# Kernel tuning notes

Measured on AMD Instinct MI355X. Metric: run time of the kernel, lower is better.

## Reference

```python
import jax, jax.numpy as jnp
import numpy as np
from jax import lax

D, NH, T, DFF, SD = 8, 4, 60, 2048, 17
DH = D // NH
NEG = -1e9

def _ln(x, g, b, eps=1e-5):
    m = jnp.mean(x, -1, keepdims=True)
    v = jnp.mean((x - m) ** 2, -1, keepdims=True)
    return (x - m) / jnp.sqrt(v + eps) * g + b

def _mha(q_in, k_in, v_in, Wqkv, bqkv, Wo, bo, mask):
    Wq, Wk, Wv = jnp.split(Wqkv, 3, axis=0)
    bq, bk, bv = jnp.split(bqkv, 3)
    def proj(x, W, bb):
        B, S, _ = x.shape
        return (x @ W.T + bb).reshape(B, S, NH, DH).transpose(0, 2, 1, 3)
    q = proj(q_in, Wq, bq); k = proj(k_in, Wk, bk); v = proj(v_in, Wv, bv)
    s = jnp.einsum('bhqd,bhkd->bhqk', q, k) / np.float32(np.sqrt(DH))
    s = jnp.where(mask, NEG, s)
    o = jnp.einsum('bhqk,bhkd->bhqd', jax.nn.softmax(s, axis=-1), v)
    B, _, S, _ = o.shape
    return o.transpose(0, 2, 1, 3).reshape(B, S, D) @ Wo.T + bo

def _ffn(x, W1, b1, W2, b2):
    return jax.nn.relu(x @ W1.T + b1) @ W2.T + b2

def _forward(x, emb_W, emb_b, eqW, eqb, eoW, eob, ef1W, ef1b, ef2W, ef2b, el1g, el1b, el2g, el2b, eng, enb, dsqW, dsqb, dsoW, dsob, dcqW, dcqb, dcoW, dcob, df1W, df1b, df2W, df2b, dl1g, dl1b, dl2g, dl2b, dl3g, dl3b, dng, dnb, fc_W, fc_b):
    B = x.shape[0]
    idx = jnp.arange(T)
    causal = (idx[None, :] > idx[:, None])[None, None]  # [1,1,T,T], True = blocked

    @jax.checkpoint
    def step(buf, t):
        keymask = (idx > t)[None, None, None, :]  # positions beyond t are padding
        mem = buf
        for i in range(6):  # nn.Transformer default encoder layers
            mem = _ln(mem + _mha(mem, mem, mem, eqW[i], eqb[i], eoW[i], eob[i], keymask), el1g[i], el1b[i])
            mem = _ln(mem + _ffn(mem, ef1W[i], ef1b[i], ef2W[i], ef2b[i]), el2g[i], el2b[i])
        mem = _ln(mem, eng, enb)
        y = buf
        for i in range(2):  # decoder layers
            y = _ln(y + _mha(y, y, y, dsqW[i], dsqb[i], dsoW[i], dsob[i], causal), dl1g[i], dl1b[i])
            y = _ln(y + _mha(y, mem, mem, dcqW[i], dcqb[i], dcoW[i], dcob[i], keymask), dl2g[i], dl2b[i])
            y = _ln(y + _ffn(y, df1W[i], df1b[i], df2W[i], df2b[i]), dl3g[i], dl3b[i])
        y = _ln(y, dng, dnb)
        st = jnp.take(y, t, axis=1) @ fc_W.T + fc_b  # decoded state at last valid pos [B,17]
        buf = buf.at[:, t + 1].set(st @ emb_W.T + emb_b, mode='drop')
        return buf, st

    buf0 = jnp.zeros((B, T, D), x.dtype).at[:, 0].set(x)
    _, states = lax.scan(step, buf0, idx)
    return jnp.transpose(states, (1, 0, 2))  # [B, T, state_dim]

def setup_inputs() -> dict:
    B = 128
    keys = iter(jax.random.split(jax.random.key(0), 64))
    def W(shape):
        return jax.random.normal(next(keys), shape, jnp.float32) / np.float32(np.sqrt(shape[-1]))
    z = lambda *s: jnp.zeros(s, jnp.float32)
    o = lambda *s: jnp.ones(s, jnp.float32)
    return dict(
        quantized_eos_embedding=jax.random.normal(next(keys), (B, D), jnp.float32),
        emb_W=W((D, SD)), emb_b=z(D),
        eqW=W((6, 3 * D, D)), eqb=z(6, 3 * D), eoW=W((6, D, D)), eob=z(6, D),
        ef1W=W((6, DFF, D)), ef1b=z(6, DFF), ef2W=W((6, D, DFF)), ef2b=z(6, D),
        el1g=o(6, D), el1b=z(6, D), el2g=o(6, D), el2b=z(6, D), eng=o(D), enb=z(D),
        dsqW=W((2, 3 * D, D)), dsqb=z(2, 3 * D), dsoW=W((2, D, D)), dsob=z(2, D),
        dcqW=W((2, 3 * D, D)), dcqb=z(2, 3 * D), dcoW=W((2, D, D)), dcob=z(2, D),
        df1W=W((2, DFF, D)), df1b=z(2, DFF), df2W=W((2, D, DFF)), df2b=z(2, D),
        dl1g=o(2, D), dl1b=z(2, D), dl2g=o(2, D), dl2b=z(2, D), dl3g=o(2, D), dl3b=z(2, D),
        dng=o(D), dnb=z(D),
        fc_W=W((SD, D)), fc_b=z(SD),
    )

def reference(quantized_eos_embedding, emb_W, emb_b, eqW, eqb, eoW, eob, ef1W, ef1b, ef2W, ef2b, el1g, el1b, el2g, el2b, eng, enb, dsqW, dsqb, dsoW, dsob, dcqW, dcqb, dcoW, dcob, df1W, df1b, df2W, df2b, dl1g, dl1b, dl2g, dl2b, dl3g, dl3b, dng, dnb, fc_W, fc_b):
    return _forward(quantized_eos_embedding, emb_W, emb_b, eqW, eqb, eoW, eob, ef1W, ef1b, ef2W, ef2b, el1g, el1b, el2g, el2b, eng, enb, dsqW, dsqb, dsoW, dsob, dcqW, dcqb, dcoW, dcob, df1W, df1b, df2W, df2b, dl1g, dl1b, dl2g, dl2b, dl3g, dl3b, dng, dnb, fc_W, fc_b)
```

## Files before the change

### kernel.cpp

```cpp
#include <hip/hip_runtime.h>


typedef __attribute__((ext_vector_type(8))) short short8;
typedef __attribute__((ext_vector_type(4))) float floatx4;
typedef __attribute__((ext_vector_type(4))) unsigned uint4v;

#define DEV static __device__ __forceinline__

namespace {
constexpr int D   = 8;
constexpr int T   = 60;
constexpr int DFF = 2048;
constexpr int SD  = 17;
constexpr int NT  = 512;
constexpr int NW  = NT / 64;
constexpr int NBLK = DFF / 32;
constexpr int BPW  = NBLK / NW;
constexpr int LSTR = NBLK * 2048;
}

struct Params { const float* in[39]; float* out; };

DEV unsigned short f2bf(float f) {
  unsigned u = __builtin_bit_cast(unsigned, f);
  return (unsigned short)((u + 0x8000u) >> 16);
}
DEV float bf2f(unsigned short h) {
  unsigned u = ((unsigned)h) << 16;
  return __builtin_bit_cast(float, u);
}
DEV floatx4 mfma16(short8 a, short8 b, floatx4 c) {
  return __builtin_amdgcn_mfma_f32_16x16x32_bf16(a, b, c, 0, 0, 0);
}
DEV unsigned cvtpk(float lo, float hi) {
  unsigned r;
  asm("v_cvt_pk_bf16_f32 %0, %1, %2" : "=v"(r) : "v"(lo), "v"(hi));
  return r;
}
DEV float lo2f(unsigned u) { return __builtin_bit_cast(float, u << 16); }
DEV float hi2f(unsigned u) { return __builtin_bit_cast(float, u & 0xffff0000u); }
DEV short8 pack4(unsigned a, unsigned b, unsigned c, unsigned d) {
  uint4v u = {a, b, c, d};
  return __builtin_bit_cast(short8, u);
}

__global__ __launch_bounds__(64) void repack_kernel(Params P, short* ws) {
  const int wg = blockIdx.x;
  const int L = wg >> 6, blk = wg & 63;
  const int l = (int)threadIdx.x, gg = l >> 4, rr = l & 15;
  const float *W1p, *b1p, *W2p;
  if (L < 6) { W1p = P.in[7] + L * 16384;  b1p = P.in[8] + L * 2048;  W2p = P.in[9] + L * 16384; }
  else { int m = L - 6; W1p = P.in[25] + m * 16384; b1p = P.in[26] + m * 2048; W2p = P.in[27] + m * 16384; }
  short* out = ws + (L * 64 + blk) * 2048;
  const int j0 = blk * 32;
  short8 z = {0,0,0,0,0,0,0,0};
  for (int tt = 0; tt < 2; ++tt) {
    int j = j0 + tt * 16 + rr;
    short8 r = z;
    if (gg == 3) {
      unsigned short h = f2bf(b1p[j]);
      r[0] = (short)h; r[1] = (short)f2bf(b1p[j] - bf2f(h));
    } else {
      const float* p = W1p + j * 8;
#pragma unroll
      for (int i = 0; i < 8; ++i) {
        float v = p[i];
        unsigned short h = f2bf(v);
        r[i] = (short)((gg == 1) ? f2bf(v - bf2f(h)) : h);
      }
    }
    *(short8*)(out + tt * 512 + l * 8) = r;
  }
  short8 wh = z, wl = z;
  if (rr < 8) {
#pragma unroll
    for (int i = 0; i < 8; ++i) {
      int j = j0 + (i < 4 ? gg * 4 + i : 16 + gg * 4 + (i - 4));
      float v = W2p[rr * 2048 + j];
      unsigned short h = f2bf(v);
      wh[i] = (short)h;
      wl[i] = (short)f2bf(v - bf2f(h));
    }
  }
  *(short8*)(out + 1024 + l * 8) = wh;
  *(short8*)(out + 1536 + l * 8) = wl;
}

__global__ __launch_bounds__(NT, 2) void tdec_kernel(Params P, const short* ws) {
  const int b    = blockIdx.x;
  const int tid  = (int)threadIdx.x;
  const int lane = tid & 63;
  const int wave = tid >> 6;
  const int gg   = lane >> 4;
  const int rr   = lane & 15;

  __shared__ float buf[T][D];
  __shared__ __align__(16) float X[64][D];
  __shared__ float Mem[64][D];
  __shared__ float Qs[64][D];
  __shared__ float Ks[64][D];
  __shared__ float Vs[64][D];
  __shared__ float ATT[64][D];
  __shared__ __align__(16) float red[NW * 1024];
  __shared__ float wAll[10 * 288];
  __shared__ float lnp[40][D];
  __shared__ float b2all[8][D];
  __shared__ float fcw[SD][D];
  __shared__ float fcbv[SD];
  __shared__ float embw[D][SD];
  __shared__ float embbv[D];
  __shared__ float stv[SD];

  for (int o = tid; o < 2880; o += NT) {
    int a = o / 288, off = o - a * 288;
    const float *Wq, *Bq, *Wo, *Bo; int li;
    if (a < 6)              { li = a;            Wq=P.in[3];  Bq=P.in[4];  Wo=P.in[5];  Bo=P.in[6];  }
    else if (((a - 6) & 1) == 0) { li = (a-6)>>1; Wq=P.in[17]; Bq=P.in[18]; Wo=P.in[19]; Bo=P.in[20]; }
    else                    { li = (a-6)>>1;     Wq=P.in[21]; Bq=P.in[22]; Wo=P.in[23]; Bo=P.in[24]; }
    float v;
    if (off < 192)      v = Wq[li*192 + off];
    else if (off < 216) v = Bq[li*24  + off - 192];
    else if (off < 280) v = Wo[li*64  + off - 216];
    else                v = Bo[li*8   + off - 280];
    wAll[o] = v;
  }
  for (int o = tid; o < 320; o += NT) {
    int row = o >> 3, k = o & 7;
    const float* src;
    if (row < 24) { int li = row >> 2, w = row & 3;
      src = (w==0 ? P.in[11] : w==1 ? P.in[12] : w==2 ? P.in[13] : P.in[14]) + li*8;
    } else if (row < 26) src = (row == 24 ? P.in[15] : P.in[16]);
    else if (row < 38) { int q = row - 26, li = q / 6, w = q - li*6;
      src = (w==0?P.in[29]:w==1?P.in[30]:w==2?P.in[31]:w==3?P.in[32]:w==4?P.in[33]:P.in[34]) + li*8;
    } else src = (row == 38 ? P.in[35] : P.in[36]);
    lnp[row][k] = src[k];
  }
  if (tid < 64) { int row = tid >> 3, k = tid & 7;
    b2all[row][k] = (row < 6) ? P.in[10][row*8 + k] : P.in[28][(row-6)*8 + k]; }
  if (tid < 136) fcw[tid >> 3][tid & 7] = P.in[37][tid];
  if (tid < SD)  fcbv[tid] = P.in[38][tid];
  if (tid < 136) embw[tid / 17][tid % 17] = P.in[1][tid];
  if (tid < D)   embbv[tid] = P.in[2][tid];
  if (tid < D)   buf[0][tid] = P.in[0][b*D + tid];
  __syncthreads();

  const short8 zero8 = {0,0,0,0,0,0,0,0};
  const floatx4 zf4  = {0.f,0.f,0.f,0.f};

  auto proj8 = [&](float (*dst)[D], const float (*src)[D], const float* w,
                   const float* bias, int R) {
    for (int o = tid; o < (R << 3); o += NT) {
      int r = o >> 3, d = o & 7;
      const float* wr = w + d * 8;
      const float* xr = src[r];
      float s = bias[d];
#pragma unroll
      for (int k = 0; k < 8; ++k) s += xr[k] * wr[k];
      dst[r][d] = s;
    }
  };

  auto attn = [&](int R, bool causal) {
    int p = tid >> 3, h2 = ((tid >> 1) & 3) << 1, e = tid & 1;
    if (p < R) {
      float q0 = Qs[p][h2]     * 0.70710678118654752f;
      float q1 = Qs[p][h2 + 1] * 0.70710678118654752f;
      int lim = causal ? p : (R - 1);
      float l = 0.f, a0 = 0.f, a1 = 0.f;
      for (int j = e; j <= lim; j += 2) {
        float s = q0 * Ks[j][h2] + q1 * Ks[j][h2 + 1] - 10.f;
        float ev = __expf(s);
        l += ev; a0 += ev * Vs[j][h2]; a1 += ev * Vs[j][h2 + 1];
      }
      l  += __shfl_xor(l, 1);
      a0 += __shfl_xor(a0, 1);
      a1 += __shfl_xor(a1, 1);
      if (e == 0) {
        float rl = 1.f / l;
        ATT[p][h2] = a0 * rl; ATT[p][h2 + 1] = a1 * rl;
      }
    }
  };

  auto oproj_ln = [&](const float* wo, const float* bo, const float* g,
                      const float* bb, int R) {
    if (tid < R) {
      float o[8];
#pragma unroll
      for (int d = 0; d < 8; ++d) {
        float s = bo[d] + X[tid][d];
#pragma unroll
        for (int k = 0; k < 8; ++k) s += ATT[tid][k] * wo[d * 8 + k];
        o[d] = s;
      }
      float m = 0.f;
#pragma unroll
      for (int k = 0; k < 8; ++k) m += o[k];
      m *= 0.125f;
      float v = 0.f;
#pragma unroll
      for (int k = 0; k < 8; ++k) { float dm = o[k] - m; v += dm * dm; }
      float rs = rsqrtf(v * 0.125f + 1e-5f);
#pragma unroll
      for (int k = 0; k < 8; ++k) X[tid][k] = (o[k] - m) * rs * g[k] + bb[k];
    }
  };

  auto ln_rows = [&](float (*dst)[D], const float (*src)[D], const float* g,
                     const float* bb, int R) {
    if (tid < R) {
      float o[8];
#pragma unroll
      for (int k = 0; k < 8; ++k) o[k] = src[tid][k];
      float m = 0.f;
#pragma unroll
      for (int k = 0; k < 8; ++k) m += o[k];
      m *= 0.125f;
      float v = 0.f;
#pragma unroll
      for (int k = 0; k < 8; ++k) { float dm = o[k] - m; v += dm * dm; }
      float rs = rsqrtf(v * 0.125f + 1e-5f);
#pragma unroll
      for (int k = 0; k < 8; ++k) dst[tid][k] = (o[k] - m) * rs * g[k] + bb[k];
    }
  };

  auto mha = [&](int a, float (*kvsrc)[D], bool causal, int R,
                 const float* g, const float* bb) {
    const float* wq = &wAll[a * 288];
    proj8(Qs, X,     wq +   0, wq + 192, R);
    proj8(Ks, kvsrc, wq +  64, wq + 200, R);
    proj8(Vs, kvsrc, wq + 128, wq + 208, R);
    __syncthreads();
    attn(R, causal);
    __syncthreads();
    oproj_ln(wq + 216, wq + 280, g, bb, R);
    __syncthreads();
  };

  auto ffn = [&](const short* wsL, const float* b2, const float* g,
                 const float* bb, int R, int Mt) {
    const short* pb = wsL + (wave * BPW) * 2048;
    short8 a0  = *(const short8*)(pb + lane * 8);
    short8 a1  = *(const short8*)(pb + 512 + lane * 8);
    short8 w2h = *(const short8*)(pb + 1024 + lane * 8);
    short8 w2l = *(const short8*)(pb + 1536 + lane * 8);

    short8 bx[4];
#pragma unroll
    for (int mt = 0; mt < 4; ++mt) {
      short8 v = zero8;
      if (mt < Mt) {
        if (gg == 3) { v[0] = (short)0x3F80; v[1] = (short)0x3F80; }
        else {
          int r = mt * 16 + rr;
          float4 A = *(const float4*)&X[r][0];
          float4 Bv = *(const float4*)&X[r][4];
          unsigned u0 = cvtpk(A.x, A.y), u1 = cvtpk(A.z, A.w);
          unsigned u2 = cvtpk(Bv.x, Bv.y), u3 = cvtpk(Bv.z, Bv.w);
          if (gg == 2) {
            unsigned l0 = cvtpk(A.x - lo2f(u0), A.y - hi2f(u0));
            unsigned l1 = cvtpk(A.z - lo2f(u1), A.w - hi2f(u1));
            unsigned l2 = cvtpk(Bv.x - lo2f(u2), Bv.y - hi2f(u2));
            unsigned l3 = cvtpk(Bv.z - lo2f(u3), Bv.w - hi2f(u3));
            v = pack4(l0, l1, l2, l3);
          } else {
            v = pack4(u0, u1, u2, u3);
          }
        }
      }
      bx[mt] = v;
    }

    floatx4 acc[4] = {zf4, zf4, zf4, zf4};
    for (int blkI = 0; blkI < BPW; ++blkI) {
      short8 na0 = zero8, na1 = zero8, nw2h = zero8, nw2l = zero8;
      if (blkI + 1 < BPW) {
        const short* pn = pb + (blkI + 1) * 2048;
        na0  = *(const short8*)(pn + lane * 8);
        na1  = *(const short8*)(pn + 512 + lane * 8);
        nw2h = *(const short8*)(pn + 1024 + lane * 8);
        nw2l = *(const short8*)(pn + 1536 + lane * 8);
      }
#pragma unroll
      for (int mt = 0; mt < 4; ++mt) {
        if (mt < Mt) {
          floatx4 h0 = mfma16(a0, bx[mt], zf4);
          floatx4 h1 = mfma16(a1, bx[mt], zf4);
          float v0 = fmaxf(h0[0], 0.f), v1 = fmaxf(h0[1], 0.f);
          float v2 = fmaxf(h0[2], 0.f), v3 = fmaxf(h0[3], 0.f);
          float v4 = fmaxf(h1[0], 0.f), v5 = fmaxf(h1[1], 0.f);
          float v6 = fmaxf(h1[2], 0.f), v7 = fmaxf(h1[3], 0.f);
          unsigned u0 = cvtpk(v0, v1), u1 = cvtpk(v2, v3);
          unsigned u2 = cvtpk(v4, v5), u3 = cvtpk(v6, v7);
          unsigned l0 = cvtpk(v0 - lo2f(u0), v1 - hi2f(u0));
          unsigned l1 = cvtpk(v2 - lo2f(u1), v3 - hi2f(u1));
          unsigned l2 = cvtpk(v4 - lo2f(u2), v5 - hi2f(u2));
          unsigned l3 = cvtpk(v6 - lo2f(u3), v7 - hi2f(u3));
          short8 ah = pack4(u0, u1, u2, u3);
          short8 al = pack4(l0, l1, l2, l3);
          acc[mt] = mfma16(w2h, ah, acc[mt]);
          acc[mt] = mfma16(w2h, al, acc[mt]);
          acc[mt] = mfma16(w2l, ah, acc[mt]);
        }
      }
      a0 = na0; a1 = na1; w2h = nw2h; w2l = nw2l;
    }

#pragma unroll
    for (int mt = 0; mt < 4; ++mt)
      if (mt < Mt)
        *(floatx4*)&red[(((wave << 2) + mt) << 8) + (lane << 2)] = acc[mt];
    __syncthreads();
    if (tid < R) {
      int r = tid, mt = r >> 4, rl = r & 15;
      float o[8];
#pragma unroll
      for (int d = 0; d < 8; ++d) {
        float s = X[r][d] + b2[d];
        int base = (mt << 8) + ((((d >> 2) << 4) + rl) << 2) + (d & 3);
#pragma unroll
        for (int w = 0; w < NW; ++w) s += red[(w << 10) + base];
        o[d] = s;
      }
      float m = 0.f;
#pragma unroll
      for (int k = 0; k < 8; ++k) m += o[k];
      m *= 0.125f;
      float var = 0.f;
#pragma unroll
      for (int k = 0; k < 8; ++k) { float dm = o[k] - m; var += dm * dm; }
      float rs = rsqrtf(var * 0.125f + 1e-5f);
#pragma unroll
      for (int k = 0; k < 8; ++k) X[r][k] = (o[k] - m) * rs * g[k] + bb[k];
    }
    __syncthreads();
  };

  for (int t = 0; t < T; ++t) {
    const int R = t + 1;
    const int Mt = (R + 15) >> 4;

    for (int o = tid; o < 512; o += NT) {
      int r = o >> 3, d = o & 7;
      X[r][d] = (r < R) ? buf[r][d] : 0.f;
    }
    __syncthreads();

    for (int li = 0; li < 6; ++li) {
      mha(li, X, false, R, lnp[li * 4 + 0], lnp[li * 4 + 1]);
      ffn(ws + li * LSTR, b2all[li], lnp[li * 4 + 2], lnp[li * 4 + 3], R, Mt);
    }
    ln_rows(X, X, lnp[24], lnp[25], R);
    __syncthreads();
    for (int o = tid; o < 512; o += NT) {
      int r = o >> 3, d = o & 7;
      if (r < R) Mem[r][d] = X[r][d];
      X[r][d] = (r < R) ? buf[r][d] : 0.f;
    }
    __syncthreads();

    for (int li = 0; li < 2; ++li) {
      mha(6 + li * 2, X,   true,  R, lnp[26 + li * 6 + 0], lnp[26 + li * 6 + 1]);
      mha(7 + li * 2, Mem, false, R, lnp[26 + li * 6 + 2], lnp[26 + li * 6 + 3]);
      ffn(ws + (6 + li) * LSTR, b2all[6 + li],
          lnp[26 + li * 6 + 4], lnp[26 + li * 6 + 5], R, Mt);
    }
    ln_rows(X, X, lnp[38], lnp[39], R);
    __syncthreads();

    if (tid < SD) {
      float s = fcbv[tid];
#pragma unroll
      for (int k = 0; k < 8; ++k) s += X[t][k] * fcw[tid][k];
      stv[tid] = s;
      P.out[(b * T + t) * SD + tid] = s;
    }
    __syncthreads();
    if (t + 1 < T && tid < D) {
      float s = embbv[tid];
#pragma unroll
      for (int k = 0; k < SD; ++k) s += stv[k] * embw[tid][k];
      buf[t + 1][tid] = s;
    }
    __syncthreads();
  }
}

extern "C" void kernel_launch(void* const* d_in, const int* in_sizes, int n_in,
                              void* d_out, int out_size, void* d_ws, size_t ws_size,
                              hipStream_t stream) {
  (void)in_sizes; (void)n_in; (void)ws_size; (void)out_size;
  Params P;
  for (int i = 0; i < 39; ++i) P.in[i] = (const float*)d_in[i];
  P.out = (float*)d_out;
  short* ws = (short*)d_ws;
  repack_kernel<<<dim3(8 * NBLK), dim3(64), 0, stream>>>(P, ws);
  tdec_kernel<<<dim3(128), dim3(NT), 0, stream>>>(P, ws);
}
```

Baseline: 3.659 ms.

## Parallelize layernorms across lanes, prefetch FFN weights two blocks ahead, widen attention

Layernorm, output projection and FFN residual-norm now use 8 lanes per row with shuffle reductions instead of one thread per row. FFN weight fragments are loaded before the output projection and kept two blocks ahead in the loop, so global loads overlap the attention epilogue. For short sequences attention splits each query over 4 lanes instead of 2, and the final fc projection is spread across lanes. This targets serial per-row work and load latency, at the cost of more registers held live for the prefetched fragments.

```diff
diff --git a/kernel.cpp b/kernel.cpp
--- a/kernel.cpp
+++ b/kernel.cpp
@@ -85,6 +85,8 @@
   *(short8*)(out + 1024 + l * 8) = wh;
   *(short8*)(out + 1536 + l * 8) = wl;
 }
+
+struct FragBlk { short8 a0, a1, w2h, w2l; };
 
 __global__ __launch_bounds__(NT, 2) void tdec_kernel(Params P, const short* ws) {
   const int b    = blockIdx.x;
@@ -147,6 +149,15 @@
   const short8 zero8 = {0,0,0,0,0,0,0,0};
   const floatx4 zf4  = {0.f,0.f,0.f,0.f};
 
+  auto ldblk = [&](const short* pb) -> FragBlk {
+    FragBlk f;
+    f.a0  = *(const short8*)(pb + lane * 8);
+    f.a1  = *(const short8*)(pb + 512 + lane * 8);
+    f.w2h = *(const short8*)(pb + 1024 + lane * 8);
+    f.w2l = *(const short8*)(pb + 1536 + lane * 8);
+    return f;
+  };
+
   auto proj8 = [&](float (*dst)[D], const float (*src)[D], const float* w,
                    const float* bias, int R) {
     for (int o = tid; o < (R << 3); o += NT) {
@@ -161,72 +172,50 @@
   };
 
   auto attn = [&](int R, bool causal) {
-    int p = tid >> 3, h2 = ((tid >> 1) & 3) << 1, e = tid & 1;
-    if (p < R) {
-      float q0 = Qs[p][h2]     * 0.70710678118654752f;
-      float q1 = Qs[p][h2 + 1] * 0.70710678118654752f;
-      int lim = causal ? p : (R - 1);
-      float l = 0.f, a0 = 0.f, a1 = 0.f;
-      for (int j = e; j <= lim; j += 2) {
-        float s = q0 * Ks[j][h2] + q1 * Ks[j][h2 + 1] - 10.f;
-        float ev = __expf(s);
-        l += ev; a0 += ev * Vs[j][h2]; a1 += ev * Vs[j][h2 + 1];
-      }
-      l  += __shfl_xor(l, 1);
-      a0 += __shfl_xor(a0, 1);
-      a1 += __shfl_xor(a1, 1);
-      if (e == 0) {
-        float rl = 1.f / l;
-        ATT[p][h2] = a0 * rl; ATT[p][h2 + 1] = a1 * rl;
-      }
-    }
-  };
-
-  auto oproj_ln = [&](const float* wo, const float* bo, const float* g,
-                      const float* bb, int R) {
-    if (tid < R) {
-      float o[8];
-#pragma unroll
-      for (int d = 0; d < 8; ++d) {
-        float s = bo[d] + X[tid][d];
-#pragma unroll
-        for (int k = 0; k < 8; ++k) s += ATT[tid][k] * wo[d * 8 + k];
-        o[d] = s;
-      }
-      float m = 0.f;
-#pragma unroll
-      for (int k = 0; k < 8; ++k) m += o[k];
-      m *= 0.125f;
-      float v = 0.f;
-#pragma unroll
-      for (int k = 0; k < 8; ++k) { float dm = o[k] - m; v += dm * dm; }
-      float rs = rsqrtf(v * 0.125f + 1e-5f);
-#pragma unroll
-      for (int k = 0; k < 8; ++k) X[tid][k] = (o[k] - m) * rs * g[k] + bb[k];
-    }
-  };
-
-  auto ln_rows = [&](float (*dst)[D], const float (*src)[D], const float* g,
-                     const float* bb, int R) {
-    if (tid < R) {
-      float o[8];
-#pragma unroll
-      for (int k = 0; k < 8; ++k) o[k] = src[tid][k];
-      float m = 0.f;
-#pragma unroll
-      for (int k = 0; k < 8; ++k) m += o[k];
-      m *= 0.125f;
-      float v = 0.f;
-#pragma unroll
-      for (int k = 0; k < 8; ++k) { float dm = o[k] - m; v += dm * dm; }
-      float rs = rsqrtf(v * 0.125f + 1e-5f);
-#pragma unroll
-      for (int k = 0; k < 8; ++k) dst[tid][k] = (o[k] - m) * rs * g[k] + bb[k];
-    }
-  };
-
-  auto mha = [&](int a, float (*kvsrc)[D], bool causal, int R,
-                 const float* g, const float* bb) {
+    if (R <= 32) {
+      int p = tid >> 4, h2 = ((tid >> 2) & 3) << 1, e = tid & 3;
+      if (p < R) {
+        float q0 = Qs[p][h2]     * 0.70710678118654752f;
+        float q1 = Qs[p][h2 + 1] * 0.70710678118654752f;
+        int lim = causal ? p : (R - 1);
+        float l = 0.f, a0 = 0.f, a1 = 0.f;
+        for (int j = e; j <= lim; j += 4) {
+          float s = q0 * Ks[j][h2] + q1 * Ks[j][h2 + 1] - 10.f;
+          float ev = __expf(s);
+          l += ev; a0 += ev * Vs[j][h2]; a1 += ev * Vs[j][h2 + 1];
+        }
+        l  += __shfl_xor(l, 1);  l  += __shfl_xor(l, 2);
+        a0 += __shfl_xor(a0, 1); a0 += __shfl_xor(a0, 2);
+        a1 += __shfl_xor(a1, 1); a1 += __shfl_xor(a1, 2);
+        if (e == 0) {
+          float rl = 1.f / l;
+          ATT[p][h2] = a0 * rl; ATT[p][h2 + 1] = a1 * rl;
+        }
+      }
+    } else {
+      int p = tid >> 3, h2 = ((tid >> 1) & 3) << 1, e = tid & 1;
+      if (p < R) {
+        float q0 = Qs[p][h2]     * 0.70710678118654752f;
+        float q1 = Qs[p][h2 + 1] * 0.70710678118654752f;
+        int lim = causal ? p : (R - 1);
+        float l = 0.f, a0 = 0.f, a1 = 0.f;
+        for (int j = e; j <= lim; j += 2) {
+          float s = q0 * Ks[j][h2] + q1 * Ks[j][h2 + 1] - 10.f;
+          float ev = __expf(s);
+          l += ev; a0 += ev * Vs[j][h2]; a1 += ev * Vs[j][h2 + 1];
+        }
+        l  += __shfl_xor(l, 1);
+        a0 += __shfl_xor(a0, 1);
+        a1 += __shfl_xor(a1, 1);
+        if (e == 0) {
+          float rl = 1.f / l;
+          ATT[p][h2] = a0 * rl; ATT[p][h2 + 1] = a1 * rl;
+        }
+      }
+    }
+  };
+
+  auto mha_qa = [&](int a, float (*kvsrc)[D], bool causal, int R) {
     const float* wq = &wAll[a * 288];
     proj8(Qs, X,     wq +   0, wq + 192, R);
     proj8(Ks, kvsrc, wq +  64, wq + 200, R);
@@ -234,18 +223,45 @@
     __syncthreads();
     attn(R, causal);
     __syncthreads();
-    oproj_ln(wq + 216, wq + 280, g, bb, R);
-    __syncthreads();
-  };
-
-  auto ffn = [&](const short* wsL, const float* b2, const float* g,
-                 const float* bb, int R, int Mt) {
-    const short* pb = wsL + (wave * BPW) * 2048;
-    short8 a0  = *(const short8*)(pb + lane * 8);
-    short8 a1  = *(const short8*)(pb + 512 + lane * 8);
-    short8 w2h = *(const short8*)(pb + 1024 + lane * 8);
-    short8 w2l = *(const short8*)(pb + 1536 + lane * 8);
-
+  };
+
+  auto oproj_ln = [&](int a, const float* g, const float* bb, int R) {
+    int r = tid >> 3, d = tid & 7;
+    if (r < R) {
+      const float* wq = &wAll[a * 288];
+      const float* wo = wq + 216;
+      float s = wq[280 + d] + X[r][d];
+#pragma unroll
+      for (int k = 0; k < 8; ++k) s += ATT[r][k] * wo[d * 8 + k];
+      float m = s;
+      m += __shfl_xor(m, 1); m += __shfl_xor(m, 2); m += __shfl_xor(m, 4);
+      m *= 0.125f;
+      float dm = s - m;
+      float v2 = dm * dm;
+      v2 += __shfl_xor(v2, 1); v2 += __shfl_xor(v2, 2); v2 += __shfl_xor(v2, 4);
+      float rs = rsqrtf(v2 * 0.125f + 1e-5f);
+      X[r][d] = dm * rs * g[d] + bb[d];
+    }
+  };
+
+  auto ln_rows = [&](float (*dst)[D], const float (*src)[D], const float* g,
+                     const float* bb, int R) {
+    int r = tid >> 3, d = tid & 7;
+    if (r < R) {
+      float s = src[r][d];
+      float m = s;
+      m += __shfl_xor(m, 1); m += __shfl_xor(m, 2); m += __shfl_xor(m, 4);
+      m *= 0.125f;
+      float dm = s - m;
+      float v2 = dm * dm;
+      v2 += __shfl_xor(v2, 1); v2 += __shfl_xor(v2, 2); v2 += __shfl_xor(v2, 4);
+      float rs = rsqrtf(v2 * 0.125f + 1e-5f);
+      dst[r][d] = dm * rs * g[d] + bb[d];
+    }
+  };
+
+  auto ffn = [&](FragBlk f0, FragBlk f1, const short* pbw, const float* b2,
+                 const float* g, const float* bb, int R, int Mt) {
     short8 bx[4];
 #pragma unroll
     for (int mt = 0; mt < 4; ++mt) {
@@ -274,19 +290,13 @@
 
     floatx4 acc[4] = {zf4, zf4, zf4, zf4};
     for (int blkI = 0; blkI < BPW; ++blkI) {
-      short8 na0 = zero8, na1 = zero8, nw2h = zero8, nw2l = zero8;
-      if (blkI + 1 < BPW) {
-        const short* pn = pb + (blkI + 1) * 2048;
-        na0  = *(const short8*)(pn + lane * 8);
-        na1  = *(const short8*)(pn + 512 + lane * 8);
-        nw2h = *(const short8*)(pn + 1024 + lane * 8);
-        nw2l = *(const short8*)(pn + 1536 + lane * 8);
-      }
+      FragBlk f2 = f1;
+      if (blkI + 2 < BPW) f2 = ldblk(pbw + (blkI + 2) * 2048);
 #pragma unroll
       for (int mt = 0; mt < 4; ++mt) {
         if (mt < Mt) {
-          floatx4 h0 = mfma16(a0, bx[mt], zf4);
-          floatx4 h1 = mfma16(a1, bx[mt], zf4);
+          floatx4 h0 = mfma16(f0.a0, bx[mt], zf4);
+          floatx4 h1 = mfma16(f0.a1, bx[mt], zf4);
           float v0 = fmaxf(h0[0], 0.f), v1 = fmaxf(h0[1], 0.f);
           float v2 = fmaxf(h0[2], 0.f), v3 = fmaxf(h0[3], 0.f);
           float v4 = fmaxf(h1[0], 0.f), v5 = fmaxf(h1[1], 0.f);
@@ -299,12 +309,12 @@
           unsigned l3 = cvtpk(v6 - lo2f(u3), v7 - hi2f(u3));
           short8 ah = pack4(u0, u1, u2, u3);
           short8 al = pack4(l0, l1, l2, l3);
-          acc[mt] = mfma16(w2h, ah, acc[mt]);
-          acc[mt] = mfma16(w2h, al, acc[mt]);
-          acc[mt] = mfma16(w2l, ah, acc[mt]);
-        }
-      }
-      a0 = na0; a1 = na1; w2h = nw2h; w2l = nw2l;
+          acc[mt] = mfma16(f0.w2h, ah, acc[mt]);
+          acc[mt] = mfma16(f0.w2h, al, acc[mt]);
+          acc[mt] = mfma16(f0.w2l, ah, acc[mt]);
+        }
+      }
+      f0 = f1; f1 = f2;
     }
 
 #pragma unroll
@@ -312,27 +322,23 @@
       if (mt < Mt)
         *(floatx4*)&red[(((wave << 2) + mt) << 8) + (lane << 2)] = acc[mt];
     __syncthreads();
-    if (tid < R) {
-      int r = tid, mt = r >> 4, rl = r & 15;
-      float o[8];
-#pragma unroll
-      for (int d = 0; d < 8; ++d) {
+    {
+      int r = tid >> 3, d = tid & 7;
+      if (r < R) {
+        int mt = r >> 4, rl = r & 15;
+        int base = (mt << 8) + ((((d >> 2) << 4) + rl) << 2) + (d & 3);
         float s = X[r][d] + b2[d];
-        int base = (mt << 8) + ((((d >> 2) << 4) + rl) << 2) + (d & 3);
 #pragma unroll
         for (int w = 0; w < NW; ++w) s += red[(w << 10) + base];
-        o[d] = s;
-      }
-      float m = 0.f;
-#pragma unroll
-      for (int k = 0; k < 8; ++k) m += o[k];
-      m *= 0.125f;
-      float var = 0.f;
-#pragma unroll
-      for (int k = 0; k < 8; ++k) { float dm = o[k] - m; var += dm * dm; }
-      float rs = rsqrtf(var * 0.125f + 1e-5f);
-#pragma unroll
-      for (int k = 0; k < 8; ++k) X[r][k] = (o[k] - m) * rs * g[k] + bb[k];
+        float m = s;
+        m += __shfl_xor(m, 1); m += __shfl_xor(m, 2); m += __shfl_xor(m, 4);
+        m *= 0.125f;
+        float dm = s - m;
+        float v2 = dm * dm;
+        v2 += __shfl_xor(v2, 1); v2 += __shfl_xor(v2, 2); v2 += __shfl_xor(v2, 4);
+        float rs = rsqrtf(v2 * 0.125f + 1e-5f);
+        X[r][d] = dm * rs * g[d] + bb[d];
+      }
     }
     __syncthreads();
   };
@@ -348,8 +354,13 @@
     __syncthreads();
 
     for (int li = 0; li < 6; ++li) {
-      mha(li, X, false, R, lnp[li * 4 + 0], lnp[li * 4 + 1]);
-      ffn(ws + li * LSTR, b2all[li], lnp[li * 4 + 2], lnp[li * 4 + 3], R, Mt);
+      const short* pbw = ws + li * LSTR + wave * BPW * 2048;
+      mha_qa(li, X, false, R);
+      FragBlk f0 = ldblk(pbw);
+      FragBlk f1 = ldblk(pbw + 2048);
+      oproj_ln(li, lnp[li * 4 + 0], lnp[li * 4 + 1], R);
+      __syncthreads();
+      ffn(f0, f1, pbw, b2all[li], lnp[li * 4 + 2], lnp[li * 4 + 3], R, Mt);
     }
     ln_rows(X, X, lnp[24], lnp[25], R);
     __syncthreads();
@@ -361,20 +372,30 @@
     __syncthreads();
 
     for (int li = 0; li < 2; ++li) {
-      mha(6 + li * 2, X,   true,  R, lnp[26 + li * 6 + 0], lnp[26 + li * 6 + 1]);
-      mha(7 + li * 2, Mem, false, R, lnp[26 + li * 6 + 2], lnp[26 + li * 6 + 3]);
-      ffn(ws + (6 + li) * LSTR, b2all[6 + li],
+      mha_qa(6 + li * 2, X, true, R);
+      oproj_ln(6 + li * 2, lnp[26 + li * 6 + 0], lnp[26 + li * 6 + 1], R);
+      __syncthreads();
+      const short* pbw = ws + (6 + li) * LSTR + wave * BPW * 2048;
+      mha_qa(7 + li * 2, Mem, false, R);
+      FragBlk f0 = ldblk(pbw);
+      FragBlk f1 = ldblk(pbw + 2048);
+      oproj_ln(7 + li * 2, lnp[26 + li * 6 + 2], lnp[26 + li * 6 + 3], R);
+      __syncthreads();
+      ffn(f0, f1, pbw, b2all[6 + li],
           lnp[26 + li * 6 + 4], lnp[26 + li * 6 + 5], R, Mt);
     }
     ln_rows(X, X, lnp[38], lnp[39], R);
     __syncthreads();
 
-    if (tid < SD) {
-      float s = fcbv[tid];
-#pragma unroll
-      for (int k = 0; k < 8; ++k) s += X[t][k] * fcw[tid][k];
-      stv[tid] = s;
-      P.out[(b * T + t) * SD + tid] = s;
+    if (tid < 136) {
+      int s_ = tid >> 3, k = tid & 7;
+      float p = X[t][k] * fcw[s_][k];
+      p += __shfl_xor(p, 1); p += __shfl_xor(p, 2); p += __shfl_xor(p, 4);
+      if (k == 0) {
+        float v = p + fcbv[s_];
+        stv[s_] = v;
+        P.out[(b * T + t) * SD + s_] = v;
+      }
     }
     __syncthreads();
     if (t + 1 < T && tid < D) {
```

Result: slower. 3.828 ms (+4.6%).
